# Kernel optimization log

Hardware: AMD Instinct MI355X
Metric: run time of the kernel (lower is better)

The kernel has to match this reference:

```python
import jax, jax.numpy as jnp
import numpy as np

# static multi-level geometry (stride 8/16/32/64 on a 1024x1024 image)
SPATIAL_SHAPES = np.array([[128, 128], [64, 64], [32, 32], [16, 16]], dtype=np.int64)
LEVEL_START = np.array([0, 16384, 20480, 21504], dtype=np.int64)
LEN_IN = 21760
N_HEADS, N_LEVELS, N_POINTS = 8, 4, 4
D_MODEL, D_FFN = 256, 1024
N_BATCH, LEN_Q = 8, 2048
EPS = 1e-5


def layer_norm(x, g, b):
    mu = jnp.mean(x, -1, keepdims=True)
    var = jnp.mean((x - mu) ** 2, -1, keepdims=True)
    return (x - mu) * jax.lax.rsqrt(var + EPS) * g + b


def sample_level(val_l, loc_l, Hl, Wl):
    # val_l: [N, nh, Hl*Wl, dh]; loc_l: [N, nh, Lq, P, 2] normalized to [0,1]
    # bilinear, align_corners=False, zero padding (matches F.grid_sample in MSDeformAttn)
    N, nh, _, dh = val_l.shape
    Lq, P = loc_l.shape[2], loc_l.shape[3]
    x = loc_l[..., 0] * Wl - 0.5
    y = loc_l[..., 1] * Hl - 0.5
    x0 = jnp.floor(x)
    y0 = jnp.floor(y)
    wx = (x - x0)[..., None]
    wy = (y - y0)[..., None]

    def gather(xi, yi):
        valid = (xi >= 0) & (xi < Wl) & (yi >= 0) & (yi < Hl)
        xi_c = jnp.clip(xi, 0, Wl - 1).astype(jnp.int32)
        yi_c = jnp.clip(yi, 0, Hl - 1).astype(jnp.int32)
        idx = (yi_c * Wl + xi_c).reshape(N, nh, Lq * P)
        g = jnp.take_along_axis(val_l, idx[..., None], axis=2).reshape(N, nh, Lq, P, dh)
        return g * valid[..., None].astype(val_l.dtype)

    v00 = gather(x0, y0)
    v01 = gather(x0 + 1, y0)
    v10 = gather(x0, y0 + 1)
    v11 = gather(x0 + 1, y0 + 1)
    return v00 * (1 - wx) * (1 - wy) + v01 * wx * (1 - wy) + v10 * (1 - wx) * wy + v11 * wx * wy


def setup_inputs() -> dict:
    key = jax.random.key(0)
    ks = jax.random.split(key, 16)
    s = 0.02
    inp = {
        'src': jax.random.normal(ks[0], (N_BATCH, LEN_Q, D_MODEL), jnp.float32),
        'pos_embed': jax.random.normal(ks[1], (N_BATCH, LEN_Q, D_MODEL), jnp.float32),
        'memorys': jax.random.normal(ks[2], (N_BATCH, LEN_IN, D_MODEL), jnp.float32),
        'pos_memory': jax.random.normal(ks[3], (N_BATCH, LEN_IN, D_MODEL), jnp.float32),
        'reference_points': jax.random.uniform(ks[4], (N_BATCH, LEN_Q, N_LEVELS, 2), jnp.float32),
        'spatial_shapes': jnp.asarray(SPATIAL_SHAPES),
        'level_start_index': jnp.asarray(LEVEL_START),
        # MSDeformAttn params
        'W_off': jax.random.normal(ks[5], (D_MODEL, N_HEADS * N_LEVELS * N_POINTS * 2), jnp.float32) * s,
        'b_off': jax.random.normal(ks[6], (N_HEADS * N_LEVELS * N_POINTS * 2,), jnp.float32) * s,
        'W_attn': jax.random.normal(ks[7], (D_MODEL, N_HEADS * N_LEVELS * N_POINTS), jnp.float32) * s,
        'b_attn': jnp.zeros((N_HEADS * N_LEVELS * N_POINTS,), jnp.float32),
        'W_val': jax.random.normal(ks[8], (D_MODEL, D_MODEL), jnp.float32) * s,
        'b_val': jnp.zeros((D_MODEL,), jnp.float32),
        'W_out': jax.random.normal(ks[9], (D_MODEL, D_MODEL), jnp.float32) * s,
        'b_out': jnp.zeros((D_MODEL,), jnp.float32),
        # norm1
        'g1': jnp.ones((D_MODEL,), jnp.float32),
        'be1': jnp.zeros((D_MODEL,), jnp.float32),
        # FFN (default: linear -> relu -> linear, residual + LayerNorm)
        'W_ff1': jax.random.normal(ks[10], (D_MODEL, D_FFN), jnp.float32) * s,
        'b_ff1': jnp.zeros((D_FFN,), jnp.float32),
        'W_ff2': jax.random.normal(ks[11], (D_FFN, D_MODEL), jnp.float32) * s,
        'b_ff2': jnp.zeros((D_MODEL,), jnp.float32),
        'g2': jnp.ones((D_MODEL,), jnp.float32),
        'be2': jnp.zeros((D_MODEL,), jnp.float32),
    }
    return inp


def reference(src, pos_embed, memorys, pos_memory, reference_points,
              spatial_shapes, level_start_index,
              W_off, b_off, W_attn, b_attn, W_val, b_val, W_out, b_out,
              g1, be1, W_ff1, b_ff1, W_ff2, b_ff2, g2, be2):
    N, Lq, D = src.shape
    nh, L, P = N_HEADS, N_LEVELS, N_POINTS
    dh = D // nh

    q = src + pos_embed                                   # with_pos_embed(src, pos)
    v = (memorys + pos_memory) @ W_val + b_val            # value_proj: [N, Lin, D]
    v = v.reshape(N, -1, nh, dh).transpose(0, 2, 1, 3)    # [N, nh, Lin, dh]

    off = (q @ W_off + b_off).reshape(N, Lq, nh, L, P, 2)
    attn = (q @ W_attn + b_attn).reshape(N, Lq, nh, L * P)
    attn = jax.nn.softmax(attn, axis=-1).reshape(N, Lq, nh, L, P)

    # offset normalizer is (W, H) per level (static geometry)
    norm = jnp.asarray(SPATIAL_SHAPES[:, ::-1].copy(), dtype=src.dtype)
    loc = reference_points[:, :, None, :, None, :] + off / norm[None, None, None, :, None, :]
    loc = loc.transpose(0, 2, 1, 3, 4, 5)                 # [N, nh, Lq, L, P, 2]
    attn = attn.transpose(0, 2, 1, 3, 4)                  # [N, nh, Lq, L, P]

    out = jnp.zeros((N, nh, Lq, dh), src.dtype)
    for l in range(L):  # small static loop over pyramid levels
        Hl, Wl = int(SPATIAL_SHAPES[l, 0]), int(SPATIAL_SHAPES[l, 1])
        s0 = int(LEVEL_START[l])
        val_l = jax.lax.dynamic_slice_in_dim(v, s0, Hl * Wl, axis=2)
        samp = sample_level(val_l, loc[:, :, :, l], Hl, Wl)   # [N, nh, Lq, P, dh]
        out = out + jnp.einsum('nhqp,nhqpd->nhqd', attn[:, :, :, l], samp)

    out = out.transpose(0, 2, 1, 3).reshape(N, Lq, D)
    src2 = out @ W_out + b_out                            # output_proj
    x = layer_norm(src + src2, g1, be1)                   # add + norm1 (dropout=eval identity)
    h = jax.nn.relu(x @ W_ff1 + b_ff1) @ W_ff2 + b_ff2    # default FFN
    return layer_norm(x + h, g2, be2)
```

## Files before the change

### kernel.cpp

```cpp
#include <hip/hip_runtime.h>
#include <hip/hip_bf16.h>
#include <stdint.h>

typedef __attribute__((ext_vector_type(4))) float f32x4;
typedef __attribute__((ext_vector_type(8))) short bf16x8;
typedef __attribute__((ext_vector_type(8))) unsigned short u16x8;
typedef __attribute__((ext_vector_type(4))) unsigned short u16x4;

#define LEN_Q 2048
#define D_MODEL 256
#define LEN_IN 21760

static __device__ __forceinline__ unsigned short f2bf(float f) {
  unsigned int u = __float_as_uint(f);
  u += 0x7fffu + ((u >> 16) & 1u);
  return (unsigned short)(u >> 16);
}
static __device__ __forceinline__ float bf2f(unsigned int us) {
  return __uint_as_float(us << 16);
}

__global__ void tconv_k(const float* __restrict__ W, unsigned short* __restrict__ WT,
                        int K, int N, int total) {
  int i = blockIdx.x * 256 + threadIdx.x;
  if (i < total) {
    int nn = i / K, k = i - nn * K;
    WT[i] = f2bf(W[(size_t)k * N + nn]);
  }
}

__global__ void copyf_k(const float* __restrict__ a, float* __restrict__ o, int n) {
  int i = blockIdx.x * 256 + threadIdx.x;
  if (i < n) o[i] = a[i];
}

__global__ void addcvt_k(const float* __restrict__ a, const float* __restrict__ b,
                         unsigned short* __restrict__ o, int n4) {
  int i = blockIdx.x * 256 + threadIdx.x;
  if (i < n4) {
    f32x4 x = ((const f32x4*)a)[i];
    f32x4 y = ((const f32x4*)b)[i];
    u16x4 r;
#pragma unroll
    for (int j = 0; j < 4; ++j) r[j] = f2bf(x[j] + y[j]);
    ((u16x4*)o)[i] = r;
  }
}

template <bool FUSEA, int BN, int EPI>
__global__ __launch_bounds__(256) void gemm_k(
    const float* __restrict__ A1, const float* __restrict__ A2,
    const unsigned short* __restrict__ Abf,
    const unsigned short* __restrict__ BT, const float* __restrict__ bias,
    float* __restrict__ Of, unsigned short* __restrict__ Ob,
    int M, int N, int K) {
  constexpr int NF = BN / 16;
  __shared__ unsigned short As[128][32];
  __shared__ unsigned short Bs[BN][32];
  const int tid = threadIdx.x;
  const int bm0 = blockIdx.x * 128;
  const int bn0 = blockIdx.y * BN;
  const int w = tid >> 6, lane = tid & 63;
  const int lr = lane & 15;
  const int lk = (lane >> 4) << 3;

  f32x4 acc[2][NF];
#pragma unroll
  for (int f = 0; f < 2; ++f)
#pragma unroll
    for (int g = 0; g < NF; ++g) acc[f][g] = (f32x4){0.f, 0.f, 0.f, 0.f};

  const int ar = tid >> 1;
  const int ak = (tid & 1) << 4;
  constexpr int TPC = 256 / BN;
  constexpr int BKT = 32 / TPC;
  const int bcol = tid / TPC;
  const int bko = (tid % TPC) * BKT;

  for (int k0 = 0; k0 < K; k0 += 32) {
    if (FUSEA) {
      const float* pa = A1 + (size_t)(bm0 + ar) * K + k0 + ak;
      const float* pb = A2 + (size_t)(bm0 + ar) * K + k0 + ak;
#pragma unroll
      for (int h = 0; h < 2; ++h) {
        f32x4 u0 = *(const f32x4*)(pa + h * 8);
        f32x4 u1 = *(const f32x4*)(pa + h * 8 + 4);
        f32x4 v0 = *(const f32x4*)(pb + h * 8);
        f32x4 v1 = *(const f32x4*)(pb + h * 8 + 4);
        u16x8 t;
#pragma unroll
        for (int j = 0; j < 4; ++j) {
          t[j] = f2bf(u0[j] + v0[j]);
          t[4 + j] = f2bf(u1[j] + v1[j]);
        }
        *(u16x8*)&As[ar][ak + h * 8] = t;
      }
    } else {
      const unsigned short* pa = Abf + (size_t)(bm0 + ar) * K + k0 + ak;
#pragma unroll
      for (int h = 0; h < 2; ++h)
        *(u16x8*)&As[ar][ak + h * 8] = *(const u16x8*)(pa + h * 8);
    }
    {
      const unsigned short* pb = BT + (size_t)(bn0 + bcol) * K + k0 + bko;
#pragma unroll
      for (int h = 0; h < BKT / 8; ++h)
        *(u16x8*)&Bs[bcol][bko + h * 8] = *(const u16x8*)(pb + h * 8);
    }
    __syncthreads();
    bf16x8 af[2];
#pragma unroll
    for (int f = 0; f < 2; ++f)
      af[f] = *(const bf16x8*)&As[w * 32 + f * 16 + lr][lk];
#pragma unroll
    for (int g = 0; g < NF; ++g) {
      bf16x8 bv = *(const bf16x8*)&Bs[g * 16 + lr][lk];
#pragma unroll
      for (int f = 0; f < 2; ++f)
        acc[f][g] = __builtin_amdgcn_mfma_f32_16x16x32_bf16(af[f], bv, acc[f][g], 0, 0, 0);
    }
    __syncthreads();
  }
#pragma unroll
  for (int f = 0; f < 2; ++f) {
    const int rg = bm0 + w * 32 + f * 16 + ((lane >> 4) << 2);
#pragma unroll
    for (int g = 0; g < NF; ++g) {
      const int cg = bn0 + g * 16 + lr;
      const float bv = bias[cg];
#pragma unroll
      for (int r = 0; r < 4; ++r) {
        float val = acc[f][g][r] + bv;
        if (EPI == 2) val = fmaxf(val, 0.f);
        size_t o = (size_t)(rg + r) * N + cg;
        if (EPI == 1) Of[o] = val;
        else Ob[o] = f2bf(val);
      }
    }
  }
}

__global__ __launch_bounds__(128) void msda_k(
    const float* __restrict__ offattn, const float* __restrict__ refp,
    const unsigned short* __restrict__ v, unsigned short* __restrict__ out) {
  const int row = blockIdx.x;
  const int n = row >> 11;
  const int t = threadIdx.x;
  const int h = t >> 4, c2 = t & 15;
  const float* oa = offattn + (size_t)row * 384;
  const float* at = oa + 256 + h * 16;
  float lg[16];
  float mx = -1e30f;
#pragma unroll
  for (int i = 0; i < 16; ++i) { lg[i] = at[i]; mx = fmaxf(mx, lg[i]); }
  float den = 0.f;
#pragma unroll
  for (int i = 0; i < 16; ++i) { lg[i] = __expf(lg[i] - mx); den += lg[i]; }
  const float rden = 1.f / den;

  const int HL[4] = {128, 64, 32, 16};
  const int S0[4] = {0, 16384, 20480, 21504};
  float acc0 = 0.f, acc1 = 0.f;
  const unsigned short* vb = v + (size_t)n * LEN_IN * 256 + h * 32 + (c2 << 1);
#pragma unroll
  for (int l = 0; l < 4; ++l) {
    const int W = HL[l], H = HL[l];
    const float Wf = (float)W;
    const int s0 = S0[l];
    const float rx = refp[(size_t)row * 8 + l * 2 + 0];
    const float ry = refp[(size_t)row * 8 + l * 2 + 1];
#pragma unroll
    for (int p = 0; p < 4; ++p) {
      const float ox = oa[h * 32 + l * 8 + p * 2 + 0];
      const float oy = oa[h * 32 + l * 8 + p * 2 + 1];
      float x = rx * Wf + ox - 0.5f;
      float y = ry * Wf + oy - 0.5f;
      float x0f = floorf(x), y0f = floorf(y);
      float wx = x - x0f, wy = y - y0f;
      int x0 = (int)x0f, y0 = (int)y0f;
      float wgt = lg[l * 4 + p] * rden;
#pragma unroll
      for (int cy = 0; cy < 2; ++cy) {
        int yi = y0 + cy;
        float wyf = cy ? wy : (1.f - wy);
        bool vy = (yi >= 0) & (yi < H);
        int yc = min(max(yi, 0), H - 1);
#pragma unroll
        for (int cx = 0; cx < 2; ++cx) {
          int xi = x0 + cx;
          float wxf = cx ? wx : (1.f - wx);
          bool vx = (xi >= 0) & (xi < W);
          int xc = min(max(xi, 0), W - 1);
          unsigned int pv = *(const unsigned int*)(vb + (size_t)(s0 + yc * W + xc) * 256);
          float wv = (vx & vy) ? (wgt * wyf * wxf) : 0.f;
          acc0 += wv * bf2f(pv & 0xffffu);
          acc1 += wv * bf2f(pv >> 16);
        }
      }
    }
  }
  unsigned int pr = ((unsigned int)f2bf(acc1) << 16) | (unsigned int)f2bf(acc0);
  *(unsigned int*)(out + (size_t)row * 256 + h * 32 + (c2 << 1)) = pr;
}

__global__ __launch_bounds__(256) void ln_k(
    const float* __restrict__ resid, const float* __restrict__ y,
    const float* __restrict__ g, const float* __restrict__ b,
    float* __restrict__ Of, unsigned short* __restrict__ Ob) {
  const int row = blockIdx.x, t = threadIdx.x;
  const size_t idx = (size_t)row * 256 + t;
  const float v = resid[idx] + y[idx];
  __shared__ float r1[256], r2[256];
  r1[t] = v;
  r2[t] = v * v;
  __syncthreads();
#pragma unroll
  for (int s = 128; s > 0; s >>= 1) {
    if (t < s) { r1[t] += r1[t + s]; r2[t] += r2[t + s]; }
    __syncthreads();
  }
  const float mu = r1[0] * (1.f / 256.f);
  const float var = r2[0] * (1.f / 256.f) - mu * mu;
  const float o = (v - mu) * rsqrtf(var + 1e-5f) * g[t] + b[t];
  Of[idx] = o;
  if (Ob) Ob[idx] = f2bf(o);
}

extern "C" void kernel_launch(void* const* d_in, const int* in_sizes, int n_in,
                              void* d_out, int out_size, void* d_ws, size_t ws_size,
                              hipStream_t stream) {
  const float* src   = (const float*)d_in[0];
  const float* pos   = (const float*)d_in[1];
  const float* mem   = (const float*)d_in[2];
  const float* posm  = (const float*)d_in[3];
  const float* refp  = (const float*)d_in[4];
  const float* W_off = (const float*)d_in[7];
  const float* b_off = (const float*)d_in[8];
  const float* W_at  = (const float*)d_in[9];
  const float* b_at  = (const float*)d_in[10];
  const float* W_val = (const float*)d_in[11];
  const float* b_val = (const float*)d_in[12];
  const float* W_out = (const float*)d_in[13];
  const float* b_out = (const float*)d_in[14];
  const float* g1    = (const float*)d_in[15];
  const float* be1   = (const float*)d_in[16];
  const float* W_ff1 = (const float*)d_in[17];
  const float* b_ff1 = (const float*)d_in[18];
  const float* W_ff2 = (const float*)d_in[19];
  const float* b_ff2 = (const float*)d_in[20];
  const float* g2    = (const float*)d_in[21];
  const float* be2   = (const float*)d_in[22];
  float* out = (float*)d_out;

  const int R = 8 * LEN_Q;
  const int MV = 8 * LEN_IN;

  char* ws = (char*)d_ws;
  size_t woff = 0;
  auto alloc = [&](size_t bytes) {
    char* p = ws + woff;
    woff += (bytes + 255) & ~(size_t)255;
    return p;
  };
  unsigned short* WT_val = (unsigned short*)alloc(256 * 256 * 2);
  unsigned short* WT_oa  = (unsigned short*)alloc(384 * 256 * 2);
  float* b_oa            = (float*)alloc(384 * 4);
  unsigned short* WT_out = (unsigned short*)alloc(256 * 256 * 2);
  unsigned short* WT_f1  = (unsigned short*)alloc(1024 * 256 * 2);
  unsigned short* WT_f2  = (unsigned short*)alloc(256 * 1024 * 2);
  unsigned short* qb     = (unsigned short*)alloc((size_t)R * 256 * 2);
  unsigned short* vb     = (unsigned short*)alloc((size_t)MV * 256 * 2);
  float* offattn         = (float*)alloc((size_t)R * 384 * 4);
  unsigned short* attno  = (unsigned short*)alloc((size_t)R * 256 * 2);
  float* tmp             = (float*)alloc((size_t)R * 256 * 4);
  float* xf              = (float*)alloc((size_t)R * 256 * 4);
  unsigned short* xb     = (unsigned short*)alloc((size_t)R * 256 * 2);
  unsigned short* hb     = (unsigned short*)alloc((size_t)R * 1024 * 2);

  tconv_k<<<256, 256, 0, stream>>>(W_val, WT_val, 256, 256, 65536);
  tconv_k<<<256, 256, 0, stream>>>(W_off, WT_oa, 256, 256, 65536);
  tconv_k<<<128, 256, 0, stream>>>(W_at, WT_oa + 256 * 256, 256, 128, 32768);
  tconv_k<<<256, 256, 0, stream>>>(W_out, WT_out, 256, 256, 65536);
  tconv_k<<<1024, 256, 0, stream>>>(W_ff1, WT_f1, 256, 1024, 262144);
  tconv_k<<<1024, 256, 0, stream>>>(W_ff2, WT_f2, 1024, 256, 262144);
  copyf_k<<<1, 256, 0, stream>>>(b_off, b_oa, 256);
  copyf_k<<<1, 128, 0, stream>>>(b_at, b_oa + 256, 128);

  addcvt_k<<<(R * 256 / 4 + 255) / 256, 256, 0, stream>>>(src, pos, qb, R * 256 / 4);

  gemm_k<true, 256, 0><<<dim3(MV / 128, 1), 256, 0, stream>>>(
      mem, posm, nullptr, WT_val, b_val, nullptr, vb, MV, 256, 256);
  gemm_k<false, 128, 1><<<dim3(R / 128, 3), 256, 0, stream>>>(
      nullptr, nullptr, qb, WT_oa, b_oa, offattn, nullptr, R, 384, 256);
  msda_k<<<R, 128, 0, stream>>>(offattn, refp, vb, attno);
  gemm_k<false, 128, 1><<<dim3(R / 128, 2), 256, 0, stream>>>(
      nullptr, nullptr, attno, WT_out, b_out, tmp, nullptr, R, 256, 256);
  ln_k<<<R, 256, 0, stream>>>(src, tmp, g1, be1, xf, xb);
  gemm_k<false, 128, 2><<<dim3(R / 128, 8), 256, 0, stream>>>(
      nullptr, nullptr, xb, WT_f1, b_ff1, nullptr, hb, R, 1024, 256);
  gemm_k<false, 128, 1><<<dim3(R / 128, 2), 256, 0, stream>>>(
      nullptr, nullptr, hb, WT_f2, b_ff2, tmp, nullptr, R, 256, 1024);
  ln_k<<<R, 256, 0, stream>>>(xf, tmp, g2, be2, out, nullptr);
}
```

Measured before the change: 674.1 us.

## Double-buffer GEMMs with direct global-to-LDS loads, merge prep kernels, shuffle LayerNorm

Replaces the GEMM kernel with a 512-thread version. It double-buffers LDS tiles, stages bf16 operands with global_load_lds direct copies, and overlaps the next tile's loads with the current tile's MFMAs. Tile shapes are also retuned per GEMM. The six weight-transpose and two bias-copy launches are merged into one prep kernel, and the LayerNorm reduction moves from a shared-memory tree to wavefront shuffles. The aim is less global-load latency exposure, fewer barriers and less launch overhead, at the cost of doubled LDS use and higher register pressure.

```diff
diff --git a/kernel.cpp b/kernel.cpp
--- a/kernel.cpp
+++ b/kernel.cpp
@@ -20,22 +20,35 @@
   return __uint_as_float(us << 16);
 }
 
-__global__ void tconv_k(const float* __restrict__ W, unsigned short* __restrict__ WT,
-                        int K, int N, int total) {
+__global__ __launch_bounds__(256) void prep_k(
+    const float* __restrict__ Wv, const float* __restrict__ Wo,
+    const float* __restrict__ Wa, const float* __restrict__ Wu,
+    const float* __restrict__ W1, const float* __restrict__ W2,
+    const float* __restrict__ boff, const float* __restrict__ batt,
+    unsigned short* __restrict__ WTv, unsigned short* __restrict__ WToa,
+    unsigned short* __restrict__ WTu, unsigned short* __restrict__ WT1,
+    unsigned short* __restrict__ WT2, float* __restrict__ b_oa) {
   int i = blockIdx.x * 256 + threadIdx.x;
-  if (i < total) {
-    int nn = i / K, k = i - nn * K;
-    WT[i] = f2bf(W[(size_t)k * N + nn]);
-  }
-}
-
-__global__ void copyf_k(const float* __restrict__ a, float* __restrict__ o, int n) {
-  int i = blockIdx.x * 256 + threadIdx.x;
-  if (i < n) o[i] = a[i];
-}
-
-__global__ void addcvt_k(const float* __restrict__ a, const float* __restrict__ b,
-                         unsigned short* __restrict__ o, int n4) {
+  if (i < 65536) { int n = i >> 8, k = i & 255; WTv[i] = f2bf(Wv[k * 256 + n]); return; }
+  i -= 65536;
+  if (i < 65536) { int n = i >> 8, k = i & 255; WToa[i] = f2bf(Wo[k * 256 + n]); return; }
+  i -= 65536;
+  if (i < 32768) { int n = i >> 8, k = i & 255; WToa[65536 + i] = f2bf(Wa[k * 128 + n]); return; }
+  i -= 32768;
+  if (i < 65536) { int n = i >> 8, k = i & 255; WTu[i] = f2bf(Wu[k * 256 + n]); return; }
+  i -= 65536;
+  if (i < 262144) { int n = i >> 8, k = i & 255; WT1[i] = f2bf(W1[k * 1024 + n]); return; }
+  i -= 262144;
+  if (i < 262144) { int n = i >> 10, k = i & 1023; WT2[i] = f2bf(W2[k * 256 + n]); return; }
+  i -= 262144;
+  if (i < 256) { b_oa[i] = boff[i]; return; }
+  i -= 256;
+  if (i < 128) { b_oa[256 + i] = batt[i]; }
+}
+
+__global__ __launch_bounds__(256) void addcvt_k(const float* __restrict__ a,
+                                                const float* __restrict__ b,
+                                                unsigned short* __restrict__ o, int n4) {
   int i = blockIdx.x * 256 + threadIdx.x;
   if (i < n4) {
     f32x4 x = ((const f32x4*)a)[i];
@@ -47,90 +60,111 @@
   }
 }
 
-template <bool FUSEA, int BN, int EPI>
-__global__ __launch_bounds__(256) void gemm_k(
+template <int FUSEA, int BM, int BN, int EPI>
+__global__ __launch_bounds__(512) void gemm2_k(
     const float* __restrict__ A1, const float* __restrict__ A2,
     const unsigned short* __restrict__ Abf,
     const unsigned short* __restrict__ BT, const float* __restrict__ bias,
     float* __restrict__ Of, unsigned short* __restrict__ Ob,
     int M, int N, int K) {
-  constexpr int NF = BN / 16;
-  __shared__ unsigned short As[128][32];
-  __shared__ unsigned short Bs[BN][32];
+  constexpr int WR = (BM == 128) ? 4 : 2;
+  constexpr int WC = 8 / WR;
+  constexpr int MR = BM / (16 * WR);
+  constexpr int NF = BN / (16 * WC);
+  constexpr int ABYTES = BM * 64;
+  constexpr int BBYTES = BN * 64;
+  __shared__ __align__(128) unsigned short As[2][BM][32];
+  __shared__ __align__(128) unsigned short Bs[2][BN][32];
+
   const int tid = threadIdx.x;
-  const int bm0 = blockIdx.x * 128;
-  const int bn0 = blockIdx.y * BN;
   const int w = tid >> 6, lane = tid & 63;
-  const int lr = lane & 15;
-  const int lk = (lane >> 4) << 3;
-
-  f32x4 acc[2][NF];
-#pragma unroll
-  for (int f = 0; f < 2; ++f)
-#pragma unroll
-    for (int g = 0; g < NF; ++g) acc[f][g] = (f32x4){0.f, 0.f, 0.f, 0.f};
-
-  const int ar = tid >> 1;
-  const int ak = (tid & 1) << 4;
-  constexpr int TPC = 256 / BN;
-  constexpr int BKT = 32 / TPC;
-  const int bcol = tid / TPC;
-  const int bko = (tid % TPC) * BKT;
-
-  for (int k0 = 0; k0 < K; k0 += 32) {
-    if (FUSEA) {
-      const float* pa = A1 + (size_t)(bm0 + ar) * K + k0 + ak;
-      const float* pb = A2 + (size_t)(bm0 + ar) * K + k0 + ak;
-#pragma unroll
-      for (int h = 0; h < 2; ++h) {
-        f32x4 u0 = *(const f32x4*)(pa + h * 8);
-        f32x4 u1 = *(const f32x4*)(pa + h * 8 + 4);
-        f32x4 v0 = *(const f32x4*)(pb + h * 8);
-        f32x4 v1 = *(const f32x4*)(pb + h * 8 + 4);
-        u16x8 t;
-#pragma unroll
-        for (int j = 0; j < 4; ++j) {
-          t[j] = f2bf(u0[j] + v0[j]);
-          t[4 + j] = f2bf(u1[j] + v1[j]);
-        }
-        *(u16x8*)&As[ar][ak + h * 8] = t;
-      }
-    } else {
-      const unsigned short* pa = Abf + (size_t)(bm0 + ar) * K + k0 + ak;
-#pragma unroll
-      for (int h = 0; h < 2; ++h)
-        *(u16x8*)&As[ar][ak + h * 8] = *(const u16x8*)(pa + h * 8);
-    }
-    {
-      const unsigned short* pb = BT + (size_t)(bn0 + bcol) * K + k0 + bko;
-#pragma unroll
-      for (int h = 0; h < BKT / 8; ++h)
-        *(u16x8*)&Bs[bcol][bko + h * 8] = *(const u16x8*)(pb + h * 8);
-    }
+  const int wr = w / WC, wc = w % WC;
+  const int lr = lane & 15, lk = (lane >> 4) << 3;
+  const int bm0 = blockIdx.x * BM, bn0 = blockIdx.y * BN;
+
+  f32x4 acc[MR][NF];
+#pragma unroll
+  for (int m = 0; m < MR; ++m)
+#pragma unroll
+    for (int g = 0; g < NF; ++g) acc[m][g] = (f32x4){0.f, 0.f, 0.f, 0.f};
+
+  const int srow = lane >> 2;
+  const int skb = (lane & 3) << 3;
+  auto stage = [&](unsigned short* lbase, const unsigned short* gbase, int kst, int bytes_) {
+    for (int off = w * 1024; off < bytes_; off += 8192) {
+      const unsigned short* src = gbase + (size_t)((off >> 6) + srow) * kst + skb;
+      __builtin_amdgcn_global_load_lds(
+          (const __attribute__((address_space(1))) unsigned int*)src,
+          (__attribute__((address_space(3))) unsigned int*)((char*)lbase + off),
+          16, 0, 0);
+    }
+  };
+
+  const int arow = tid >> 2;
+  const int ak8 = (tid & 3) << 3;
+  f32x4 r10, r11, r20, r21;
+  auto loadA = [&](int k0) {
+    const float* p1 = A1 + (size_t)(bm0 + arow) * K + k0 + ak8;
+    const float* p2 = A2 + (size_t)(bm0 + arow) * K + k0 + ak8;
+    r10 = *(const f32x4*)p1;
+    r11 = *(const f32x4*)(p1 + 4);
+    r20 = *(const f32x4*)p2;
+    r21 = *(const f32x4*)(p2 + 4);
+  };
+  auto writeA = [&](int p) {
+    u16x8 tv;
+#pragma unroll
+    for (int j = 0; j < 4; ++j) {
+      tv[j] = f2bf(r10[j] + r20[j]);
+      tv[4 + j] = f2bf(r11[j] + r21[j]);
+    }
+    *(u16x8*)&As[p][arow][ak8] = tv;
+  };
+
+  const int NT = K >> 5;
+  stage(&Bs[0][0][0], BT + (size_t)bn0 * K, K, BBYTES);
+  if (FUSEA) {
+    loadA(0);
+    writeA(0);
+  } else {
+    stage(&As[0][0][0], Abf + (size_t)bm0 * K, K, ABYTES);
+  }
+  __syncthreads();
+
+  int p = 0;
+  for (int t = 0; t < NT; ++t) {
+    const int kn = (t + 1) << 5;
+    if (t + 1 < NT) {
+      stage(&Bs[p ^ 1][0][0], BT + (size_t)bn0 * K + kn, K, BBYTES);
+      if (FUSEA) loadA(kn);
+      else stage(&As[p ^ 1][0][0], Abf + (size_t)bm0 * K + kn, K, ABYTES);
+    }
+    bf16x8 af[MR];
+#pragma unroll
+    for (int m = 0; m < MR; ++m)
+      af[m] = *(const bf16x8*)&As[p][wr * (BM / WR) + m * 16 + lr][lk];
+#pragma unroll
+    for (int g = 0; g < NF; ++g) {
+      bf16x8 bv = *(const bf16x8*)&Bs[p][wc * (BN / WC) + g * 16 + lr][lk];
+#pragma unroll
+      for (int m = 0; m < MR; ++m)
+        acc[m][g] = __builtin_amdgcn_mfma_f32_16x16x32_bf16(af[m], bv, acc[m][g], 0, 0, 0);
+    }
+    if (FUSEA && t + 1 < NT) writeA(p ^ 1);
     __syncthreads();
-    bf16x8 af[2];
-#pragma unroll
-    for (int f = 0; f < 2; ++f)
-      af[f] = *(const bf16x8*)&As[w * 32 + f * 16 + lr][lk];
+    p ^= 1;
+  }
+
+#pragma unroll
+  for (int m = 0; m < MR; ++m) {
+    const int rg = bm0 + wr * (BM / WR) + m * 16 + ((lane >> 4) << 2);
 #pragma unroll
     for (int g = 0; g < NF; ++g) {
-      bf16x8 bv = *(const bf16x8*)&Bs[g * 16 + lr][lk];
-#pragma unroll
-      for (int f = 0; f < 2; ++f)
-        acc[f][g] = __builtin_amdgcn_mfma_f32_16x16x32_bf16(af[f], bv, acc[f][g], 0, 0, 0);
-    }
-    __syncthreads();
-  }
-#pragma unroll
-  for (int f = 0; f < 2; ++f) {
-    const int rg = bm0 + w * 32 + f * 16 + ((lane >> 4) << 2);
-#pragma unroll
-    for (int g = 0; g < NF; ++g) {
-      const int cg = bn0 + g * 16 + lr;
+      const int cg = bn0 + wc * (BN / WC) + g * 16 + lr;
       const float bv = bias[cg];
 #pragma unroll
       for (int r = 0; r < 4; ++r) {
-        float val = acc[f][g][r] + bv;
+        float val = acc[m][g][r] + bv;
         if (EPI == 2) val = fmaxf(val, 0.f);
         size_t o = (size_t)(rg + r) * N + cg;
         if (EPI == 1) Of[o] = val;
@@ -210,17 +244,19 @@
   const int row = blockIdx.x, t = threadIdx.x;
   const size_t idx = (size_t)row * 256 + t;
   const float v = resid[idx] + y[idx];
-  __shared__ float r1[256], r2[256];
-  r1[t] = v;
-  r2[t] = v * v;
+  float s1 = v, s2 = v * v;
+#pragma unroll
+  for (int d = 32; d > 0; d >>= 1) {
+    s1 += __shfl_xor(s1, d, 64);
+    s2 += __shfl_xor(s2, d, 64);
+  }
+  __shared__ float p1[4], p2[4];
+  const int w = t >> 6;
+  if ((t & 63) == 0) { p1[w] = s1; p2[w] = s2; }
   __syncthreads();
-#pragma unroll
-  for (int s = 128; s > 0; s >>= 1) {
-    if (t < s) { r1[t] += r1[t + s]; r2[t] += r2[t + s]; }
-    __syncthreads();
-  }
-  const float mu = r1[0] * (1.f / 256.f);
-  const float var = r2[0] * (1.f / 256.f) - mu * mu;
+  const float mu = (p1[0] + p1[1] + p1[2] + p1[3]) * (1.f / 256.f);
+  const float m2 = (p2[0] + p2[1] + p2[2] + p2[3]) * (1.f / 256.f);
+  const float var = m2 - mu * mu;
   const float o = (v - mu) * rsqrtf(var + 1e-5f) * g[t] + b[t];
   Of[idx] = o;
   if (Ob) Ob[idx] = f2bf(o);
@@ -277,28 +313,22 @@
   unsigned short* xb     = (unsigned short*)alloc((size_t)R * 256 * 2);
   unsigned short* hb     = (unsigned short*)alloc((size_t)R * 1024 * 2);
 
-  tconv_k<<<256, 256, 0, stream>>>(W_val, WT_val, 256, 256, 65536);
-  tconv_k<<<256, 256, 0, stream>>>(W_off, WT_oa, 256, 256, 65536);
-  tconv_k<<<128, 256, 0, stream>>>(W_at, WT_oa + 256 * 256, 256, 128, 32768);
-  tconv_k<<<256, 256, 0, stream>>>(W_out, WT_out, 256, 256, 65536);
-  tconv_k<<<1024, 256, 0, stream>>>(W_ff1, WT_f1, 256, 1024, 262144);
-  tconv_k<<<1024, 256, 0, stream>>>(W_ff2, WT_f2, 1024, 256, 262144);
-  copyf_k<<<1, 256, 0, stream>>>(b_off, b_oa, 256);
-  copyf_k<<<1, 128, 0, stream>>>(b_at, b_oa + 256, 128);
-
-  addcvt_k<<<(R * 256 / 4 + 255) / 256, 256, 0, stream>>>(src, pos, qb, R * 256 / 4);
-
-  gemm_k<true, 256, 0><<<dim3(MV / 128, 1), 256, 0, stream>>>(
+  prep_k<<<2946, 256, 0, stream>>>(W_val, W_off, W_at, W_out, W_ff1, W_ff2,
+                                   b_off, b_at, WT_val, WT_oa, WT_out, WT_f1,
+                                   WT_f2, b_oa);
+  addcvt_k<<<4096, 256, 0, stream>>>(src, pos, qb, R * 64);
+
+  gemm2_k<1, 128, 256, 0><<<dim3(MV / 128, 1), 512, 0, stream>>>(
       mem, posm, nullptr, WT_val, b_val, nullptr, vb, MV, 256, 256);
-  gemm_k<false, 128, 1><<<dim3(R / 128, 3), 256, 0, stream>>>(
+  gemm2_k<0, 64, 128, 1><<<dim3(R / 64, 3), 512, 0, stream>>>(
       nullptr, nullptr, qb, WT_oa, b_oa, offattn, nullptr, R, 384, 256);
   msda_k<<<R, 128, 0, stream>>>(offattn, refp, vb, attno);
-  gemm_k<false, 128, 1><<<dim3(R / 128, 2), 256, 0, stream>>>(
+  gemm2_k<0, 64, 256, 1><<<dim3(R / 64, 1), 512, 0, stream>>>(
       nullptr, nullptr, attno, WT_out, b_out, tmp, nullptr, R, 256, 256);
   ln_k<<<R, 256, 0, stream>>>(src, tmp, g1, be1, xf, xb);
-  gemm_k<false, 128, 2><<<dim3(R / 128, 8), 256, 0, stream>>>(
+  gemm2_k<0, 128, 256, 2><<<dim3(R / 128, 4), 512, 0, stream>>>(
       nullptr, nullptr, xb, WT_f1, b_ff1, nullptr, hb, R, 1024, 256);
-  gemm_k<false, 128, 1><<<dim3(R / 128, 2), 256, 0, stream>>>(
+  gemm2_k<0, 64, 256, 1><<<dim3(R / 64, 1), 512, 0, stream>>>(
       nullptr, nullptr, hb, WT_f2, b_ff2, tmp, nullptr, R, 256, 1024);
   ln_k<<<R, 256, 0, stream>>>(xf, tmp, g2, be2, out, nullptr);
 }
```

New measurement: 609.8 us. 9.5% less time.
